# Kernel tuning notes

Hardware: AMD Instinct MI355X
Metric: run time of the kernel (lower is better)

The kernel has to match this reference:

```python
import jax, jax.numpy as jnp
import numpy as np

N_SAMPLING = 32
N_FINAL = 8
FEATURE_DEPTH = 128
H = 128
W = 128
N_LINES = 50000


def setup_inputs() -> dict:
    key = jax.random.key(0)
    k1, k2 = jax.random.split(key)
    features_per_image = jax.random.normal(k1, (FEATURE_DEPTH, H, W), dtype=jnp.float32)
    # line endpoints in pixel coordinates, roughly spanning the feature map
    lines_per_im = jax.random.uniform(k2, (N_LINES, 4), dtype=jnp.float32) * float(W)
    return {"features_per_image": features_per_image, "lines_per_im": lines_per_im}


def reference(features_per_image, lines_per_im):
    C, h, w = features_per_image.shape
    tspan = jnp.linspace(0.0, 1.0, N_SAMPLING, dtype=jnp.float32)[None, None, :]  # [1,1,S]
    U = lines_per_im[:, :2]   # [N,2]
    V = lines_per_im[:, 2:]   # [N,2]
    # [N,2,S] -> permute -> [N*S, 2]
    sampled = U[:, :, None] * tspan + V[:, :, None] * (1.0 - tspan) - 0.5
    sampled = jnp.transpose(sampled, (0, 2, 1)).reshape(-1, 2)
    px, py = sampled[:, 0], sampled[:, 1]
    px0 = jnp.clip(jnp.floor(px), 0.0, w - 1)
    py0 = jnp.clip(jnp.floor(py), 0.0, h - 1)
    px1 = jnp.clip(px0 + 1.0, 0.0, w - 1)
    py1 = jnp.clip(py0 + 1.0, 0.0, h - 1)
    px0l, py0l = px0.astype(jnp.int32), py0.astype(jnp.int32)
    px1l, py1l = px1.astype(jnp.int32), py1.astype(jnp.int32)
    # four bilinear gathers, each [C, N*S]
    xp = (features_per_image[:, py0l, px0l] * ((py1 - py) * (px1 - px))[None, :]
          + features_per_image[:, py1l, px0l] * ((py - py0) * (px1 - px))[None, :]
          + features_per_image[:, py0l, px1l] * ((py1 - py) * (px - px0))[None, :]
          + features_per_image[:, py1l, px1l] * ((py - py0) * (px - px0))[None, :])
    # [C, N, S] -> [N, C, S]
    xp = jnp.transpose(xp.reshape(C, -1, N_SAMPLING), (1, 0, 2))
    # MaxPool1d(kernel=stride=S//F): [N, C, F, S//F] -> max over last axis
    pool = N_SAMPLING // N_FINAL
    xp = xp.reshape(xp.shape[0], C, N_FINAL, pool).max(axis=-1)
    return xp.reshape(-1, N_FINAL * FEATURE_DEPTH)
```

## Files before the change

### kernel.cpp

```cpp
#include <hip/hip_runtime.h>
#include <hip/hip_fp16.h>
#include <float.h>

#define C_DEPTH 128
#define H_DIM 128
#define W_DIM 128
#define NPIX (H_DIM * W_DIM)
#define N_SAMP 32
#define N_FINAL 8
#define N_LINES 50000

typedef float v4f __attribute__((ext_vector_type(4)));

__global__ __launch_bounds__(256) void transpose_quant(
    const float* __restrict__ in, char* __restrict__ outq,
    __half* __restrict__ scale_out) {
    __shared__ float tile[64 * 130];
    __shared__ float s_part[4][64];
    __shared__ float s_inv[64];
    const int p0 = blockIdx.x * 64;
    const int t = threadIdx.x;

    const int p_local = t & 63;
    const int cg = t >> 6;
    #pragma unroll
    for (int i = 0; i < 32; ++i) {
        const int ch = cg * 32 + i;
        tile[p_local * 130 + ch] = in[ch * NPIX + p0 + p_local];
    }
    __syncthreads();

    float m = 0.0f;
    #pragma unroll
    for (int i = 0; i < 32; ++i)
        m = fmaxf(m, fabsf(tile[p_local * 130 + cg * 32 + i]));
    s_part[cg][p_local] = m;
    __syncthreads();
    if (t < 64) {
        float mm = fmaxf(fmaxf(s_part[0][t], s_part[1][t]),
                         fmaxf(s_part[2][t], s_part[3][t]));
        mm = fmaxf(mm, 1e-3f);
        const __half h = __float2half(mm * (1.0f / 127.0f));
        const float s_r = __half2float(h);
        scale_out[p0 + t] = h;
        s_inv[t] = 1.0f / s_r;
    }
    __syncthreads();

    const int cp = (t & 63) * 2;
    const int pg = t >> 6;
    #pragma unroll
    for (int i = 0; i < 16; ++i) {
        const int p = pg * 16 + i;
        const float inv = s_inv[p];
        const float2 f2 = *reinterpret_cast<const float2*>(&tile[p * 130 + cp]);
        const int q0 = (int)rintf(f2.x * inv);
        const int q1 = (int)rintf(f2.y * inv);
        const unsigned short pk =
            (unsigned short)((q0 & 0xff) | ((q1 & 0xff) << 8));
        *reinterpret_cast<unsigned short*>(
            outq + (size_t)(p0 + p) * C_DEPTH + cp) = pk;
    }
}

__device__ __forceinline__ float sx(unsigned int w, int j) {
    return (float)((int)(w << ((3 - j) * 8)) >> 24);
}

__global__ __launch_bounds__(128) void line_pool(
    const char* __restrict__ ft,
    const __half* __restrict__ scale,
    const float* __restrict__ lines,
    float* __restrict__ out) {
    __shared__ int4   s_off[N_SAMP];
    __shared__ float4 s_w[N_SAMP];
    __shared__ float  o_tile[C_DEPTH * 9];

    const int line = blockIdx.x;
    const int t = threadIdx.x;

    if (t < N_SAMP) {
        const float4 l = reinterpret_cast<const float4*>(lines)[line];
        const float ts = (float)t / 31.0f;
        const float px = l.x * ts + l.z * (1.0f - ts) - 0.5f;
        const float py = l.y * ts + l.w * (1.0f - ts) - 0.5f;
        const float px0 = fminf(fmaxf(floorf(px), 0.0f), (float)(W_DIM - 1));
        const float py0 = fminf(fmaxf(floorf(py), 0.0f), (float)(H_DIM - 1));
        const float px1 = fminf(px0 + 1.0f, (float)(W_DIM - 1));
        const float py1 = fminf(py0 + 1.0f, (float)(H_DIM - 1));
        const int ix0 = (int)px0, iy0 = (int)py0;
        const int ix1 = (int)px1, iy1 = (int)py1;
        const float wx0 = px1 - px, wx1 = px - px0;
        const float wy0 = py1 - py, wy1 = py - py0;
        const int p00 = iy0 * W_DIM + ix0;
        const int p10 = iy1 * W_DIM + ix0;
        const int p01 = iy0 * W_DIM + ix1;
        const int p11 = iy1 * W_DIM + ix1;
        const float s00 = __half2float(scale[p00]);
        const float s10 = __half2float(scale[p10]);
        const float s01 = __half2float(scale[p01]);
        const float s11 = __half2float(scale[p11]);
        s_off[t] = make_int4(p00 * C_DEPTH, p10 * C_DEPTH,
                             p01 * C_DEPTH, p11 * C_DEPTH);
        s_w[t] = make_float4(wy0 * wx0 * s00, wy1 * wx0 * s10,
                             wy0 * wx1 * s01, wy1 * wx1 * s11);
    }
    __syncthreads();

    const int f  = t >> 4;
    const int tg = t & 15;
    const int c0 = tg * 8;

    float acc[8];
    #pragma unroll
    for (int j = 0; j < 8; ++j) acc[j] = -FLT_MAX;

    #pragma unroll
    for (int si = 0; si < 4; ++si) {
        const int4   o  = s_off[f * 4 + si];
        const float4 wv = s_w[f * 4 + si];
        const uint2 d00 = *reinterpret_cast<const uint2*>(ft + o.x + c0);
        const uint2 d10 = *reinterpret_cast<const uint2*>(ft + o.y + c0);
        const uint2 d01 = *reinterpret_cast<const uint2*>(ft + o.z + c0);
        const uint2 d11 = *reinterpret_cast<const uint2*>(ft + o.w + c0);
        #pragma unroll
        for (int j = 0; j < 8; ++j) {
            const int jj = j & 3;
            const unsigned int w00 = (j < 4) ? d00.x : d00.y;
            const unsigned int w10 = (j < 4) ? d10.x : d10.y;
            const unsigned int w01 = (j < 4) ? d01.x : d01.y;
            const unsigned int w11 = (j < 4) ? d11.x : d11.y;
            const float v = sx(w00, jj) * wv.x + sx(w10, jj) * wv.y
                          + sx(w01, jj) * wv.z + sx(w11, jj) * wv.w;
            acc[j] = fmaxf(acc[j], v);
        }
    }

    #pragma unroll
    for (int j = 0; j < 8; ++j) o_tile[(c0 + j) * 9 + f] = acc[j];
    __syncthreads();

    float* op = out + (size_t)line * (C_DEPTH * N_FINAL) + t * N_FINAL;
    const float* row = &o_tile[t * 9];
    const v4f w0 = {row[0], row[1], row[2], row[3]};
    const v4f w1 = {row[4], row[5], row[6], row[7]};
    __builtin_nontemporal_store(w0, reinterpret_cast<v4f*>(op));
    __builtin_nontemporal_store(w1, reinterpret_cast<v4f*>(op) + 1);
}

extern "C" void kernel_launch(void* const* d_in, const int* in_sizes, int n_in,
                              void* d_out, int out_size, void* d_ws, size_t ws_size,
                              hipStream_t stream) {
    const float* feat  = (const float*)d_in[0];
    const float* lines = (const float*)d_in[1];
    float* out = (float*)d_out;
    char*   ft = (char*)d_ws;
    __half* sc = (__half*)((char*)d_ws + (size_t)NPIX * C_DEPTH);

    transpose_quant<<<NPIX / 64, 256, 0, stream>>>(feat, ft, sc);
    line_pool<<<N_LINES, 128, 0, stream>>>(ft, sc, lines, out);
}
```

Measured before the change: 277.0 us.

## Fetch adjacent-pixel pairs with 16B loads staged through LDS

Instead of four 8-byte gathers per sample, each thread loads 16 bytes covering two horizontally adjacent quantized pixels (p00/p01 and p10/p11 are contiguous in the pixel-major layout) for two rows. The data is written into a per-wave double-buffered LDS stage and read back in the per-thread channel layout. At the right edge (ix1==ix0) the weights are folded into the left pixel, and a zeroed pad is added past the quantized buffer so that the overread stays in bounds. This halves the number of global gather instructions at the cost of extra LDS traffic, explicit waitcnt barriers and a block sync.

```diff
diff --git a/kernel.cpp b/kernel.cpp
--- a/kernel.cpp
+++ b/kernel.cpp
@@ -20,6 +20,9 @@
     __shared__ float s_inv[64];
     const int p0 = blockIdx.x * 64;
     const int t = threadIdx.x;
+
+    if (blockIdx.x == 0 && t < 32)
+        *reinterpret_cast<int*>(outq + (size_t)NPIX * C_DEPTH + t * 4) = 0;
 
     const int p_local = t & 63;
     const int cg = t >> 6;
@@ -72,9 +75,10 @@
     const __half* __restrict__ scale,
     const float* __restrict__ lines,
     float* __restrict__ out) {
-    __shared__ int4   s_off[N_SAMP];
+    __shared__ __align__(16) char stage[2 * 2 * 4 * 512];
+    __shared__ int2   s_pb[N_SAMP];
     __shared__ float4 s_w[N_SAMP];
-    __shared__ float  o_tile[C_DEPTH * 9];
+    float* o_tile = reinterpret_cast<float*>(stage);
 
     const int line = blockIdx.x;
     const int t = threadIdx.x;
@@ -100,16 +104,21 @@
         const float s10 = __half2float(scale[p10]);
         const float s01 = __half2float(scale[p01]);
         const float s11 = __half2float(scale[p11]);
-        s_off[t] = make_int4(p00 * C_DEPTH, p10 * C_DEPTH,
-                             p01 * C_DEPTH, p11 * C_DEPTH);
-        s_w[t] = make_float4(wy0 * wx0 * s00, wy1 * wx0 * s10,
-                             wy0 * wx1 * s01, wy1 * wx1 * s11);
+        float4 wv = make_float4(wy0 * wx0 * s00, wy1 * wx0 * s10,
+                                wy0 * wx1 * s01, wy1 * wx1 * s11);
+        if (ix1 == ix0) { wv.x += wv.z; wv.z = 0.0f; wv.y += wv.w; wv.w = 0.0f; }
+        s_pb[t] = make_int2(p00 * C_DEPTH, p10 * C_DEPTH);
+        s_w[t] = wv;
     }
     __syncthreads();
 
-    const int f  = t >> 4;
-    const int tg = t & 15;
-    const int c0 = tg * 8;
+    const int w    = t >> 6;
+    const int lane = t & 63;
+    const int fl   = lane >> 4;
+    const int slot = lane & 15;
+    const int f    = t >> 4;
+
+    char* wbase = stage + (w * 4096 + fl * 512);
 
     float acc[8];
     #pragma unroll
@@ -117,25 +126,37 @@
 
     #pragma unroll
     for (int si = 0; si < 4; ++si) {
-        const int4   o  = s_off[f * 4 + si];
-        const float4 wv = s_w[f * 4 + si];
-        const uint2 d00 = *reinterpret_cast<const uint2*>(ft + o.x + c0);
-        const uint2 d10 = *reinterpret_cast<const uint2*>(ft + o.y + c0);
-        const uint2 d01 = *reinterpret_cast<const uint2*>(ft + o.z + c0);
-        const uint2 d11 = *reinterpret_cast<const uint2*>(ft + o.w + c0);
+        const int smp = f * 4 + si;
+        const int2 pb = s_pb[smp];
+        const v4f d0 = *reinterpret_cast<const v4f*>(ft + pb.x + slot * 16);
+        const v4f d1 = *reinterpret_cast<const v4f*>(ft + pb.y + slot * 16);
+        char* bp = wbase + (si & 1) * 2048;
+        *reinterpret_cast<v4f*>(bp + slot * 16)       = d0;
+        *reinterpret_cast<v4f*>(bp + 256 + slot * 16) = d1;
+        asm volatile("s_waitcnt lgkmcnt(0)" ::: "memory");
+        __builtin_amdgcn_sched_barrier(0);
+
+        const float4 wv = s_w[smp];
+        const uint2 d00 = *reinterpret_cast<const uint2*>(bp +       slot * 8);
+        const uint2 d01 = *reinterpret_cast<const uint2*>(bp + 128 + slot * 8);
+        const uint2 d10 = *reinterpret_cast<const uint2*>(bp + 256 + slot * 8);
+        const uint2 d11 = *reinterpret_cast<const uint2*>(bp + 384 + slot * 8);
         #pragma unroll
         for (int j = 0; j < 8; ++j) {
             const int jj = j & 3;
-            const unsigned int w00 = (j < 4) ? d00.x : d00.y;
-            const unsigned int w10 = (j < 4) ? d10.x : d10.y;
-            const unsigned int w01 = (j < 4) ? d01.x : d01.y;
-            const unsigned int w11 = (j < 4) ? d11.x : d11.y;
-            const float v = sx(w00, jj) * wv.x + sx(w10, jj) * wv.y
-                          + sx(w01, jj) * wv.z + sx(w11, jj) * wv.w;
+            const unsigned int b00 = (j < 4) ? d00.x : d00.y;
+            const unsigned int b01 = (j < 4) ? d01.x : d01.y;
+            const unsigned int b10 = (j < 4) ? d10.x : d10.y;
+            const unsigned int b11 = (j < 4) ? d11.x : d11.y;
+            const float v = sx(b00, jj) * wv.x + sx(b10, jj) * wv.y
+                          + sx(b01, jj) * wv.z + sx(b11, jj) * wv.w;
             acc[j] = fmaxf(acc[j], v);
         }
     }
 
+    __syncthreads();
+
+    const int c0 = slot * 8;
     #pragma unroll
     for (int j = 0; j < 8; ++j) o_tile[(c0 + j) * 9 + f] = acc[j];
     __syncthreads();
@@ -155,7 +176,7 @@
     const float* lines = (const float*)d_in[1];
     float* out = (float*)d_out;
     char*   ft = (char*)d_ws;
-    __half* sc = (__half*)((char*)d_ws + (size_t)NPIX * C_DEPTH);
+    __half* sc = (__half*)((char*)d_ws + (size_t)NPIX * C_DEPTH + 256);
 
     transpose_quant<<<NPIX / 64, 256, 0, stream>>>(feat, ft, sc);
     line_pool<<<N_LINES, 128, 0, stream>>>(ft, sc, lines, out);
```

Result: faster. 244.1 us (-11.9%).
